# Kernel tuning notes

Hardware: AMD Instinct MI355X
Metric: run time of the kernel (lower is better)

Reference implementation:

```python
import jax, jax.numpy as jnp
import numpy as np

MODEL_DIM = 512
NUM_HEADS = 8
HEAD_DIM = MODEL_DIM // NUM_HEADS  # 64
NUM_NODE = 1024
CLUSTER = 128
S = 60
EMBED = 0.5


def setup_inputs() -> dict:
    key = jax.random.key(0)
    ks = jax.random.split(key, 16)
    d = MODEL_DIM
    sc = 1.0 / np.sqrt(d)
    inp = {
        "x": jax.random.normal(ks[0], (4, 12, NUM_NODE, d), dtype=jnp.float32),
        "Wq": jax.random.normal(ks[1], (d, d), dtype=jnp.float32) * sc,
        "bq": jnp.zeros((d,), jnp.float32),
        "Wk": jax.random.normal(ks[2], (d, d), dtype=jnp.float32) * sc,
        "bk": jnp.zeros((d,), jnp.float32),
        "Wv": jax.random.normal(ks[3], (d, d), dtype=jnp.float32) * sc,
        "bv": jnp.zeros((d,), jnp.float32),
        "We": jax.random.normal(ks[4], (d, d), dtype=jnp.float32) * sc,
        "be": jnp.zeros((d,), jnp.float32),
        "Wo": jax.random.normal(ks[5], (d, d), dtype=jnp.float32) * sc,
        "bo": jnp.zeros((d,), jnp.float32),
        # adp_pos is initialized to zeros in torch; use small randn for a non-degenerate test
        "adp_pos": jax.random.normal(ks[6], (NUM_NODE, CLUSTER), dtype=jnp.float32) * 0.02,
        "U1": jax.random.normal(ks[7], (HEAD_DIM, S), dtype=jnp.float32) * np.sqrt(2.0 / (HEAD_DIM + S)),
        "U2": jax.random.normal(ks[8], (S, HEAD_DIM), dtype=jnp.float32) * np.sqrt(2.0 / (S + HEAD_DIM)),
    }
    return inp


def _split_heads(t):
    # torch.cat(torch.split(t, head_dim, -1), 0): heads stacked head-major on batch dim
    return jnp.concatenate(jnp.split(t, NUM_HEADS, axis=-1), axis=0)


def _merge_heads(t):
    return jnp.concatenate(jnp.split(t, NUM_HEADS, axis=0), axis=-1)


def _pool_nodes(t):
    # AdaptiveAvgPool2d((CLUSTER, None)) on (B,T,N,D) with N % CLUSTER == 0 -> block mean
    B, T, N, D = t.shape
    return t.reshape(B, T, CLUSTER, N // CLUSTER, D).mean(axis=3)


def reference(x, Wq, bq, Wk, bk, Wv, bv, We, be, Wo, bo, adp_pos, U1, U2):
    q = x @ Wq.T + bq                      # (B,T,N,D)
    k = _pool_nodes(x @ Wk.T + bk)          # (B,T,C,D)
    v = _pool_nodes(x @ Wv.T + bv)          # (B,T,C,D)
    ev = x @ We.T + be                      # (B,T,N,D)

    qh = _split_heads(q)                    # (B*H,T,N,d)
    kh = _split_heads(k)                    # (B*H,T,C,d)
    vh = _split_heads(v)                    # (B*H,T,C,d)
    evh = _split_heads(ev)                  # (B*H,T,N,d)

    # external attention branch: softmax over node dim (-2)
    exa = jax.nn.softmax(evh @ U1, axis=-2)  # (B*H,T,N,S)
    exa_val = (exa @ U2) * EMBED + evh       # (B*H,T,N,d)

    score = jnp.einsum("btnd,btcd->btnc", qh, kh) / np.sqrt(HEAD_DIM)
    score = score + adp_pos[None, None]      # (B*H,T,N,C)
    attn = jax.nn.softmax(score, axis=-1)

    out = attn @ vh + exa_val                # (B*H,T,N,d)
    out = _merge_heads(out)                  # (B,T,N,D)
    return out @ Wo.T + bo
```

## Files before the change

kernel.cpp:

```cpp
#include <hip/hip_runtime.h>


#define LOG2E 1.44269504088896f

typedef __attribute__((ext_vector_type(4))) float f32x4;
typedef __attribute__((ext_vector_type(8))) short bf16x8;

__device__ __forceinline__ unsigned short f2bf(float f) {
    union { float f; unsigned u; } v; v.f = f;
    unsigned r = (v.u + 0x7fffu + ((v.u >> 16) & 1u)) >> 16;
    return (unsigned short)r;
}
__device__ __forceinline__ float bf2f(unsigned short h) {
    union { unsigned u; float f; } v; v.u = ((unsigned)h) << 16;
    return v.f;
}
__device__ __forceinline__ unsigned cvt_pk_bf16(float lo, float hi) {
    unsigned r;
    asm("v_cvt_pk_bf16_f32 %0, %1, %2" : "=v"(r) : "v"(lo), "v"(hi));
    return r;
}
__device__ __forceinline__ void gll16(const void* g, void* l) {
    __builtin_amdgcn_global_load_lds((const __attribute__((address_space(1))) void*)g,
                                     (__attribute__((address_space(3))) void*)l,
                                     16, 0, 0);
}

__global__ void cvt_w(const float* __restrict__ Wq, const float* __restrict__ Wk,
                      const float* __restrict__ Wv, const float* __restrict__ We,
                      const float* __restrict__ Wo, const float* __restrict__ U1,
                      const float* __restrict__ U2,
                      const float* __restrict__ bq, const float* __restrict__ bk,
                      const float* __restrict__ bv, const float* __restrict__ be,
                      unsigned short* __restrict__ Wqe, unsigned short* __restrict__ Wkv,
                      unsigned short* __restrict__ Wob, unsigned short* __restrict__ U1T,
                      unsigned short* __restrict__ U2bT,
                      float* __restrict__ bqe, float* __restrict__ bkv)
{
    int i = blockIdx.x * 256 + threadIdx.x;
    if (i < 524288) {
        int r = i >> 9;
        float v = (r < 512) ? Wq[i] * 0.125f : We[i - 262144];
        Wqe[i] = f2bf(v);
    } else if (i < 1048576) {
        int j = i - 524288; int r = j >> 9;
        float v = (r < 512) ? Wk[j] : Wv[j - 262144];
        Wkv[j] = f2bf(v);
    } else if (i < 1310720) {
        int j = i - 1048576;
        Wob[j] = f2bf(Wo[j]);
    } else if (i < 1314816) {
        int j = i - 1310720; int s = j >> 6, k = j & 63;
        U1T[j] = (s < 60) ? f2bf(U1[k * 60 + s] * LOG2E) : (unsigned short)0;
    } else if (i < 1318912) {
        int j = i - 1314816; int d = j >> 6, s = j & 63;
        U2bT[j] = (s < 60) ? f2bf(U2[s * 64 + d] * 0.5f) : (unsigned short)0;
    } else if (i < 1319936) {
        int j = i - 1318912;
        bqe[j] = (j < 512) ? bq[j] * 0.125f : be[j - 512];
    } else if (i < 1320960) {
        int j = i - 1319936;
        bkv[j] = (j < 512) ? bk[j] : bv[j - 512];
    }
}

__global__ void cvt_pool(const float* __restrict__ x, unsigned short* __restrict__ xb,
                         unsigned short* __restrict__ xpb)
{
    int i = blockIdx.x * 256 + threadIdx.x;
    int d4 = i & 127;
    int btc = i >> 7;
    int bt = btc >> 7, c = btc & 127;
    long base = ((long)(bt * 1024 + c * 8)) * 128 + d4;
    const float4* src = (const float4*)x + base;
    ushort4* dst = (ushort4*)xb + base;
    float sx = 0.f, sy = 0.f, sz = 0.f, sw = 0.f;
#pragma unroll
    for (int j = 0; j < 8; j++) {
        float4 v = src[(long)j * 128];
        sx += v.x; sy += v.y; sz += v.z; sw += v.w;
        ushort4 o;
        o.x = f2bf(v.x); o.y = f2bf(v.y); o.z = f2bf(v.z); o.w = f2bf(v.w);
        dst[(long)j * 128] = o;
    }
    ushort4 p;
    p.x = f2bf(sx * 0.125f); p.y = f2bf(sy * 0.125f);
    p.z = f2bf(sz * 0.125f); p.w = f2bf(sw * 0.125f);
    ((ushort4*)xpb)[(long)btc * 128 + d4] = p;
}

__global__ __launch_bounds__(256, 4) void g1_qev(
    const unsigned short* __restrict__ A, const unsigned short* __restrict__ W,
    const float* __restrict__ bias, unsigned short* __restrict__ qh,
    unsigned short* __restrict__ evh)
{
    const int K = 512;
    __shared__ __attribute__((aligned(16))) unsigned short As[128 * 32];
    __shared__ __attribute__((aligned(16))) unsigned short Bs[128 * 32];
    const int tid = threadIdx.x;
    const int wave = tid >> 6, lane = tid & 63;
    const int quad = lane >> 4, l16 = lane & 15;
    const int b = blockIdx.x, xcd = b & 7, j = b >> 3;
    const int m0 = (((j >> 3) << 3) + xcd) * 128, n0 = (j & 7) * 128;
    const int wm = (wave & 1) * 64, wn = (wave >> 1) * 64;

    f32x4 acc[4][4];
#pragma unroll
    for (int i = 0; i < 4; i++)
#pragma unroll
        for (int jj = 0; jj < 4; jj++) acc[i][jj] = (f32x4){0.f, 0.f, 0.f, 0.f};

    const int c0 = tid, c1 = tid + 256;
    const int r0 = c0 >> 2, kc0 = (c0 & 3) * 8;
    const int r1 = c1 >> 2, kc1 = (c1 & 3) * 8;
    const unsigned short* pa0 = A + (long)(m0 + r0) * K + kc0;
    const unsigned short* pa1 = A + (long)(m0 + r1) * K + kc1;
    const unsigned short* pb0 = W + (long)(n0 + r0) * K + kc0;
    const unsigned short* pb1 = W + (long)(n0 + r1) * K + kc1;
    unsigned short* lA0 = &As[wave * 512];
    unsigned short* lA1 = &As[2048 + wave * 512];
    unsigned short* lB0 = &Bs[wave * 512];
    unsigned short* lB1 = &Bs[2048 + wave * 512];

    for (int k0 = 0; k0 < K; k0 += 32) {
        gll16(pa0 + k0, lA0);
        gll16(pa1 + k0, lA1);
        gll16(pb0 + k0, lB0);
        gll16(pb1 + k0, lB1);
        __syncthreads();
        bf16x8 af[4], bfr[4];
#pragma unroll
        for (int t = 0; t < 4; t++)
            af[t] = *(const bf16x8*)&As[(wm + t * 16 + l16) * 32 + quad * 8];
#pragma unroll
        for (int t = 0; t < 4; t++)
            bfr[t] = *(const bf16x8*)&Bs[(wn + t * 16 + l16) * 32 + quad * 8];
#pragma unroll
        for (int tm = 0; tm < 4; tm++)
#pragma unroll
            for (int tn = 0; tn < 4; tn++)
                acc[tm][tn] = __builtin_amdgcn_mfma_f32_16x16x32_bf16(
                    af[tm], bfr[tn], acc[tm][tn], 0, 0, 0);
        __syncthreads();
    }

#pragma unroll
    for (int tm = 0; tm < 4; tm++)
#pragma unroll
        for (int tn = 0; tn < 4; tn++) {
            int cc = n0 + wn + tn * 16 + l16;
            float bv = bias[cc];
            int hq = (cc >> 6) & 7, dd = cc & 63;
            int rr0 = m0 + wm + tm * 16 + quad * 4;
            int bt = rr0 >> 10, n = rr0 & 1023;
            unsigned short* dst = ((cc < 512) ? qh : evh)
                + ((long)(bt * 8 + hq) * 1024 + n) * 64 + dd;
#pragma unroll
            for (int r = 0; r < 4; r++)
                dst[(long)r * 64] = f2bf(acc[tm][tn][r] + bv);
        }
}

template <int NTL2>
__global__ __launch_bounds__(256, 4) void gemm_bt(
    const unsigned short* __restrict__ A, const unsigned short* __restrict__ W,
    const float* __restrict__ bias, float* __restrict__ Cout,
    int N, int K)
{
    __shared__ __attribute__((aligned(16))) unsigned short As[128 * 32];
    __shared__ __attribute__((aligned(16))) unsigned short Bs[128 * 32];
    const int tid = threadIdx.x;
    const int wave = tid >> 6, lane = tid & 63;
    const int quad = lane >> 4, l16 = lane & 15;
    const int b = blockIdx.x, xcd = b & 7, j = b >> 3;
    const int m0 = (((j >> NTL2) << 3) + xcd) * 128;
    const int n0 = (j & ((1 << NTL2) - 1)) * 128;
    const int wm = (wave & 1) * 64, wn = (wave >> 1) * 64;

    f32x4 acc[4][4];
#pragma unroll
    for (int i = 0; i < 4; i++)
#pragma unroll
        for (int jj = 0; jj < 4; jj++) acc[i][jj] = (f32x4){0.f, 0.f, 0.f, 0.f};

    const int c0 = tid, c1 = tid + 256;
    const int r0 = c0 >> 2, kc0 = (c0 & 3) * 8;
    const int r1 = c1 >> 2, kc1 = (c1 & 3) * 8;
    const unsigned short* pa0 = A + (long)(m0 + r0) * K + kc0;
    const unsigned short* pa1 = A + (long)(m0 + r1) * K + kc1;
    const unsigned short* pb0 = W + (long)(n0 + r0) * K + kc0;
    const unsigned short* pb1 = W + (long)(n0 + r1) * K + kc1;
    unsigned short* lA0 = &As[wave * 512];
    unsigned short* lA1 = &As[2048 + wave * 512];
    unsigned short* lB0 = &Bs[wave * 512];
    unsigned short* lB1 = &Bs[2048 + wave * 512];

    for (int k0 = 0; k0 < K; k0 += 32) {
        gll16(pa0 + k0, lA0);
        gll16(pa1 + k0, lA1);
        gll16(pb0 + k0, lB0);
        gll16(pb1 + k0, lB1);
        __syncthreads();
        bf16x8 af[4], bfr[4];
#pragma unroll
        for (int t = 0; t < 4; t++)
            af[t] = *(const bf16x8*)&As[(wm + t * 16 + l16) * 32 + quad * 8];
#pragma unroll
        for (int t = 0; t < 4; t++)
            bfr[t] = *(const bf16x8*)&Bs[(wn + t * 16 + l16) * 32 + quad * 8];
#pragma unroll
        for (int tm = 0; tm < 4; tm++)
#pragma unroll
            for (int tn = 0; tn < 4; tn++)
                acc[tm][tn] = __builtin_amdgcn_mfma_f32_16x16x32_bf16(
                    af[tm], bfr[tn], acc[tm][tn], 0, 0, 0);
        __syncthreads();
    }

#pragma unroll
    for (int tm = 0; tm < 4; tm++)
#pragma unroll
        for (int tn = 0; tn < 4; tn++) {
            int cc = n0 + wn + tn * 16 + l16;
            float bv = bias[cc];
#pragma unroll
            for (int r = 0; r < 4; r++) {
                int rr = m0 + wm + tm * 16 + quad * 4 + r;
                Cout[(long)rr * N + cc] = acc[tm][tn][r] + bv;
            }
        }
}

__global__ __launch_bounds__(256, 4) void g2_kv(
    const unsigned short* __restrict__ A, const unsigned short* __restrict__ W,
    const float* __restrict__ bias, unsigned short* __restrict__ kvK,
    unsigned short* __restrict__ vT)
{
    const int K = 512;
    __shared__ __attribute__((aligned(16))) unsigned short As[128 * 32];
    __shared__ __attribute__((aligned(16))) unsigned short Bs[128 * 32];
    const int tid = threadIdx.x;
    const int wave = tid >> 6, lane = tid & 63;
    const int quad = lane >> 4, l16 = lane & 15;
    const int b = blockIdx.x, xcd = b & 7, j = b >> 3;
    const int m0 = (((j >> 3) << 3) + xcd) * 128, n0 = (j & 7) * 128;
    const int wm = (wave & 1) * 64, wn = (wave >> 1) * 64;

    f32x4 acc[4][4];
#pragma unroll
    for (int i = 0; i < 4; i++)
#pragma unroll
        for (int jj = 0; jj < 4; jj++) acc[i][jj] = (f32x4){0.f, 0.f, 0.f, 0.f};

    const int c0 = tid, c1 = tid + 256;
    const int r0 = c0 >> 2, kc0 = (c0 & 3) * 8;
    const int r1 = c1 >> 2, kc1 = (c1 & 3) * 8;
    const unsigned short* pa0 = A + (long)(m0 + r0) * K + kc0;
    const unsigned short* pa1 = A + (long)(m0 + r1) * K + kc1;
    const unsigned short* pb0 = W + (long)(n0 + r0) * K + kc0;
    const unsigned short* pb1 = W + (long)(n0 + r1) * K + kc1;
    unsigned short* lA0 = &As[wave * 512];
    unsigned short* lA1 = &As[2048 + wave * 512];
    unsigned short* lB0 = &Bs[wave * 512];
    unsigned short* lB1 = &Bs[2048 + wave * 512];

    for (int k0 = 0; k0 < K; k0 += 32) {
        gll16(pa0 + k0, lA0);
        gll16(pa1 + k0, lA1);
        gll16(pb0 + k0, lB0);
        gll16(pb1 + k0, lB1);
        __syncthreads();
        bf16x8 af[4], bfr[4];
#pragma unroll
        for (int t = 0; t < 4; t++)
            af[t] = *(const bf16x8*)&As[(wm + t * 16 + l16) * 32 + quad * 8];
#pragma unroll
        for (int t = 0; t < 4; t++)
            bfr[t] = *(const bf16x8*)&Bs[(wn + t * 16 + l16) * 32 + quad * 8];
#pragma unroll
        for (int tm = 0; tm < 4; tm++)
#pragma unroll
            for (int tn = 0; tn < 4; tn++)
                acc[tm][tn] = __builtin_amdgcn_mfma_f32_16x16x32_bf16(
                    af[tm], bfr[tn], acc[tm][tn], 0, 0, 0);
        __syncthreads();
    }

#pragma unroll
    for (int tm = 0; tm < 4; tm++)
#pragma unroll
        for (int tn = 0; tn < 4; tn++) {
            int cc = n0 + wn + tn * 16 + l16;
            float bv = bias[cc];
            int rrb = m0 + wm + tm * 16 + quad * 4;
            if (cc < 512) {
#pragma unroll
                for (int r = 0; r < 4; r++)
                    kvK[(long)(rrb + r) * 512 + cc] = f2bf(acc[tm][tn][r] + bv);
            } else {
                int hh = (cc - 512) >> 6, dd = (cc - 512) & 63;
                int btv = rrb >> 7, cv = rrb & 127;
                ushort4 o;
                o.x = f2bf(acc[tm][tn][0] + bv);
                o.y = f2bf(acc[tm][tn][1] + bv);
                o.z = f2bf(acc[tm][tn][2] + bv);
                o.w = f2bf(acc[tm][tn][3] + bv);
                *(ushort4*)(vT + ((long)(btv * 8 + hh) * 64 + dd) * 128 + cv) = o;
            }
        }
}

__global__ __launch_bounds__(256, 4) void ez_kernel(
    const unsigned short* __restrict__ evh, const unsigned short* __restrict__ U1T,
    float* __restrict__ pM, float* __restrict__ pL)
{
    __shared__ float ms4[4][64];
    __shared__ float ls4[4][64];
    int tid = threadIdx.x, bx = blockIdx.x;
    int bt = bx >> 6, h = (bx >> 3) & 7, nb = bx & 7;
    int wave = tid >> 6, lane = tid & 63, quad = lane >> 4, l16 = lane & 15;
    long gb0 = (long)(bt * 8 + h) * 1024 + nb * 128;

    f32x4 acc[2][4];
#pragma unroll
    for (int i = 0; i < 2; i++)
#pragma unroll
        for (int t = 0; t < 4; t++) acc[i][t] = (f32x4){0.f, 0.f, 0.f, 0.f};

#pragma unroll
    for (int kt = 0; kt < 2; kt++) {
        bf16x8 a[2], b[4];
#pragma unroll
        for (int i = 0; i < 2; i++)
            a[i] = *(const bf16x8*)(evh + (gb0 + (wave * 2 + i) * 16 + l16) * 64
                                    + kt * 32 + quad * 8);
#pragma unroll
        for (int t = 0; t < 4; t++)
            b[t] = *(const bf16x8*)(U1T + (t * 16 + l16) * 64 + kt * 32 + quad * 8);
#pragma unroll
        for (int i = 0; i < 2; i++)
#pragma unroll
            for (int t = 0; t < 4; t++)
                acc[i][t] = __builtin_amdgcn_mfma_f32_16x16x32_bf16(a[i], b[t], acc[i][t], 0, 0, 0);
    }

    float mp[4], lp[4];
#pragma unroll
    for (int t = 0; t < 4; t++) {
        float m = -1e30f;
#pragma unroll
        for (int i = 0; i < 2; i++)
#pragma unroll
            for (int r = 0; r < 4; r++) m = fmaxf(m, acc[i][t][r]);
        float l = 0.f;
#pragma unroll
        for (int i = 0; i < 2; i++)
#pragma unroll
            for (int r = 0; r < 4; r++) l += exp2f(acc[i][t][r] - m);
        mp[t] = m; lp[t] = l;
    }
#pragma unroll
    for (int d = 16; d <= 32; d <<= 1)
#pragma unroll
        for (int t = 0; t < 4; t++) {
            float mo = __shfl_xor(mp[t], d, 64);
            float lo = __shfl_xor(lp[t], d, 64);
            float nm = fmaxf(mp[t], mo);
            lp[t] = lp[t] * exp2f(mp[t] - nm) + lo * exp2f(mo - nm);
            mp[t] = nm;
        }
    if (quad == 0) {
#pragma unroll
        for (int t = 0; t < 4; t++) {
            ms4[wave][t * 16 + l16] = mp[t];
            ls4[wave][t * 16 + l16] = lp[t];
        }
    }
    __syncthreads();
    if (tid < 64) {
        float M = ms4[0][tid];
#pragma unroll
        for (int w = 1; w < 4; w++) M = fmaxf(M, ms4[w][tid]);
        float L = 0.f;
#pragma unroll
        for (int w = 0; w < 4; w++) L += ls4[w][tid] * exp2f(ms4[w][tid] - M);
        pM[(long)bx * 64 + tid] = M;
        pL[(long)bx * 64 + tid] = L;
    }
}

__global__ void es_reduce(const float* __restrict__ pM, const float* __restrict__ pL,
                          float* __restrict__ dS)
{
    int g = blockIdx.x, s = threadIdx.x;
    float mv[8], lv[8], M = -1e30f;
#pragma unroll
    for (int nb = 0; nb < 8; nb++) {
        mv[nb] = pM[(long)(g * 8 + nb) * 64 + s];
        lv[nb] = pL[(long)(g * 8 + nb) * 64 + s];
        M = fmaxf(M, mv[nb]);
    }
    float L = 0.f;
#pragma unroll
    for (int nb = 0; nb < 8; nb++) L += lv[nb] * exp2f(mv[nb] - M);
    dS[(long)g * 64 + s] = (s < 60) ? (M + __log2f(L)) : 1e30f;
}

__global__ __launch_bounds__(256, 4) void att_kernel(
    const unsigned short* __restrict__ qh, const unsigned short* __restrict__ evh,
    const unsigned short* __restrict__ kvK, const unsigned short* __restrict__ vT,
    const float* __restrict__ dS, const float* __restrict__ adp,
    const unsigned short* __restrict__ U1T, const unsigned short* __restrict__ U2bT,
    unsigned short* __restrict__ attn_out)
{
    __shared__ __attribute__((aligned(16))) unsigned short Ps[128 * 136];

    int tid = threadIdx.x, bx = blockIdx.x;
    int bt = bx >> 6, h = (bx >> 3) & 7, nb = bx & 7;
    int wave = tid >> 6, lane = tid & 63, quad = lane >> 4, l16 = lane & 15;
    int n0 = nb * 128;
    const int g = bt * 8 + h;
    const long grow0 = (long)g * 1024 + n0;

    f32x4 sc[2][8];
#pragma unroll
    for (int i = 0; i < 2; i++)
#pragma unroll
        for (int t = 0; t < 8; t++) sc[i][t] = (f32x4){0.f, 0.f, 0.f, 0.f};

#pragma unroll
    for (int kt = 0; kt < 2; kt++) {
        bf16x8 qf[2];
#pragma unroll
        for (int i = 0; i < 2; i++)
            qf[i] = *(const bf16x8*)(qh + (grow0 + wave * 32 + i * 16 + l16) * 64
                                     + kt * 32 + quad * 8);
#pragma unroll
        for (int tn = 0; tn < 8; tn++) {
            bf16x8 kf = *(const bf16x8*)(kvK + (long)(bt * 128 + tn * 16 + l16) * 512
                                         + h * 64 + kt * 32 + quad * 8);
#pragma unroll
            for (int i = 0; i < 2; i++)
                sc[i][tn] = __builtin_amdgcn_mfma_f32_16x16x32_bf16(kf, qf[i], sc[i][tn], 0, 0, 0);
        }
    }

#pragma unroll
    for (int i = 0; i < 2; i++) {
        const int qr = wave * 32 + i * 16 + l16;
        float m = -1e30f;
#pragma unroll
        for (int tn = 0; tn < 8; tn++) {
            float4 ad = *(const float4*)(adp + (long)(n0 + qr) * 128 + tn * 16 + quad * 4);
            sc[i][tn][0] += ad.x; sc[i][tn][1] += ad.y;
            sc[i][tn][2] += ad.z; sc[i][tn][3] += ad.w;
#pragma unroll
            for (int r = 0; r < 4; r++) m = fmaxf(m, sc[i][tn][r]);
        }
        m = fmaxf(m, __shfl_xor(m, 16, 64));
        m = fmaxf(m, __shfl_xor(m, 32, 64));
        float s = 0.f;
#pragma unroll
        for (int tn = 0; tn < 8; tn++)
#pragma unroll
            for (int r = 0; r < 4; r++) {
                float p = exp2f((sc[i][tn][r] - m) * LOG2E);
                sc[i][tn][r] = p; s += p;
            }
        s += __shfl_xor(s, 16, 64);
        s += __shfl_xor(s, 32, 64);
        float rinv = 1.0f / s;
#pragma unroll
        for (int tn = 0; tn < 8; tn++) {
            uint2 w2;
            w2.x = cvt_pk_bf16(sc[i][tn][0] * rinv, sc[i][tn][1] * rinv);
            w2.y = cvt_pk_bf16(sc[i][tn][2] * rinv, sc[i][tn][3] * rinv);
            *(uint2*)&Ps[qr * 136 + tn * 16 + quad * 4] = w2;
        }
    }

    f32x4 za[2][4];
#pragma unroll
    for (int i = 0; i < 2; i++)
#pragma unroll
        for (int t = 0; t < 4; t++) za[i][t] = (f32x4){0.f, 0.f, 0.f, 0.f};
#pragma unroll
    for (int kt = 0; kt < 2; kt++) {
        bf16x8 u1f[4], evf[2];
#pragma unroll
        for (int t = 0; t < 4; t++)
            u1f[t] = *(const bf16x8*)(U1T + (t * 16 + l16) * 64 + kt * 32 + quad * 8);
#pragma unroll
        for (int i = 0; i < 2; i++)
            evf[i] = *(const bf16x8*)(evh + (grow0 + wave * 32 + i * 16 + l16) * 64
                                      + kt * 32 + quad * 8);
#pragma unroll
        for (int i = 0; i < 2; i++)
#pragma unroll
            for (int t = 0; t < 4; t++)
                za[i][t] = __builtin_amdgcn_mfma_f32_16x16x32_bf16(u1f[t], evf[i], za[i][t], 0, 0, 0);
    }
    float4 dv[4];
#pragma unroll
    for (int t = 0; t < 4; t++)
        dv[t] = *(const float4*)(dS + (long)g * 64 + t * 16 + quad * 4);

    f32x4 oc[2][4];
#pragma unroll
    for (int i = 0; i < 2; i++)
#pragma unroll
        for (int t = 0; t < 4; t++) oc[i][t] = (f32x4){0.f, 0.f, 0.f, 0.f};

#pragma unroll
    for (int kt = 0; kt < 4; kt++) {
        bf16x8 a[2];
#pragma unroll
        for (int i = 0; i < 2; i++)
            a[i] = *(const bf16x8*)&Ps[(wave * 32 + i * 16 + l16) * 136 + kt * 32 + quad * 8];
#pragma unroll
        for (int tn = 0; tn < 4; tn++) {
            bf16x8 b = *(const bf16x8*)(vT + ((long)g * 64 + tn * 16 + l16) * 128
                                        + kt * 32 + quad * 8);
#pragma unroll
            for (int i = 0; i < 2; i++)
                oc[i][tn] = __builtin_amdgcn_mfma_f32_16x16x32_bf16(a[i], b, oc[i][tn], 0, 0, 0);
        }
    }

#pragma unroll
    for (int i = 0; i < 2; i++) {
        const int row = wave * 32 + i * 16 + l16;
#pragma unroll
        for (int t = 0; t < 4; t++) {
            float e0 = exp2f(za[i][t][0] - dv[t].x);
            float e1 = exp2f(za[i][t][1] - dv[t].y);
            float e2 = exp2f(za[i][t][2] - dv[t].z);
            float e3 = exp2f(za[i][t][3] - dv[t].w);
            uint2 w2;
            w2.x = cvt_pk_bf16(e0, e1);
            w2.y = cvt_pk_bf16(e2, e3);
            *(uint2*)&Ps[row * 136 + t * 16 + quad * 4] = w2;
        }
    }

#pragma unroll
    for (int kt = 0; kt < 2; kt++) {
        bf16x8 eaf[2];
#pragma unroll
        for (int i = 0; i < 2; i++)
            eaf[i] = *(const bf16x8*)&Ps[(wave * 32 + i * 16 + l16) * 136 + kt * 32 + quad * 8];
#pragma unroll
        for (int tn = 0; tn < 4; tn++) {
            bf16x8 b = *(const bf16x8*)(U2bT + (tn * 16 + l16) * 64 + kt * 32 + quad * 8);
#pragma unroll
            for (int i = 0; i < 2; i++)
                oc[i][tn] = __builtin_amdgcn_mfma_f32_16x16x32_bf16(eaf[i], b, oc[i][tn], 0, 0, 0);
        }
    }

#pragma unroll
    for (int i = 0; i < 2; i++)
#pragma unroll
        for (int tn = 0; tn < 4; tn++)
#pragma unroll
            for (int r = 0; r < 4; r++) {
                int rr = wave * 32 + i * 16 + quad * 4 + r;
                int cc = tn * 16 + l16;
                float ev = bf2f(evh[(grow0 + rr) * 64 + cc]);
                attn_out[((long)bt * 1024 + n0 + rr) * 512 + h * 64 + cc]
                    = f2bf(oc[i][tn][r] + ev);
            }
}

extern "C" void kernel_launch(void* const* d_in, const int* in_sizes, int n_in,
                              void* d_out, int out_size, void* d_ws, size_t ws_size,
                              hipStream_t stream)
{
    const float* x   = (const float*)d_in[0];
    const float* Wq  = (const float*)d_in[1];
    const float* bq  = (const float*)d_in[2];
    const float* Wk  = (const float*)d_in[3];
    const float* bk  = (const float*)d_in[4];
    const float* Wv  = (const float*)d_in[5];
    const float* bv  = (const float*)d_in[6];
    const float* We  = (const float*)d_in[7];
    const float* be  = (const float*)d_in[8];
    const float* Wo  = (const float*)d_in[9];
    const float* bo  = (const float*)d_in[10];
    const float* adp = (const float*)d_in[11];
    const float* U1  = (const float*)d_in[12];
    const float* U2  = (const float*)d_in[13];

    char* ws = (char*)d_ws;
    unsigned short* xb   = (unsigned short*)(ws + 0);
    unsigned short* aout = xb;
    float*          pMb  = (float*)(ws + 0);
    float*          pLb  = (float*)(ws + 786432);
    unsigned short* xpb  = (unsigned short*)(ws + 50331648);
    unsigned short* qh   = (unsigned short*)(ws + 56623104);
    unsigned short* evh  = (unsigned short*)(ws + 106954752);
    unsigned short* kvK  = (unsigned short*)(ws + 157286400);
    unsigned short* vT   = (unsigned short*)(ws + 163577856);
    float*          dSb  = (float*)(ws + 169869312);
    unsigned short* Wqe  = (unsigned short*)(ws + 217055232);
    unsigned short* Wkv  = (unsigned short*)(ws + 218103808);
    unsigned short* Wob  = (unsigned short*)(ws + 219152384);
    unsigned short* U1T  = (unsigned short*)(ws + 219676672);
    unsigned short* U2bT = (unsigned short*)(ws + 219684864);
    float*          bqe  = (float*)(ws + 219877376);
    float*          bkv  = (float*)(ws + 219881472);

    cvt_w<<<5160, 256, 0, stream>>>(Wq, Wk, Wv, We, Wo, U1, U2, bq, bk, bv, be,
                                    Wqe, Wkv, Wob, U1T, U2bT, bqe, bkv);
    cvt_pool<<<3072, 256, 0, stream>>>(x, xb, xpb);

    g1_qev<<<3072, 256, 0, stream>>>(xb, Wqe, bqe, qh, evh);
    g2_kv<<<384, 256, 0, stream>>>(xpb, Wkv, bkv, kvK, vT);

    ez_kernel<<<3072, 256, 0, stream>>>(evh, U1T, pMb, pLb);
    es_reduce<<<384, 64, 0, stream>>>(pMb, pLb, dSb);
    att_kernel<<<3072, 256, 0, stream>>>(qh, evh, kvK, vT, dSb, adp, U1T, U2bT, aout);

    gemm_bt<2><<<1536, 256, 0, stream>>>(aout, Wob, bo, (float*)d_out, 512, 512);
}
```

Before: 446.1 us.

## Double GEMM K-tile to 64 with XOR-swizzled LDS and hoist evh loads

The three bf16 GEMM kernels now stage a 64-wide K tile per iteration instead of 32. This halves the number of barrier pairs and loop iterations. An XOR swizzle on the column chunk, applied both in the global-to-LDS load addressing and the fragment reads, is meant to avoid LDS bank conflicts from the wider 128-byte rows. The attention kernel now issues its evh fragment loads earlier, before the softmax, so their latency overlaps with that work. In exchange LDS use per block doubles, which may cut occupancy, and the early loads keep more registers live.

Measured after the change: 463.8 us. 1.04x slower.

```diff
diff --git a/kernel.cpp b/kernel.cpp
--- a/kernel.cpp
+++ b/kernel.cpp
@@ -89,14 +89,15 @@
     ((ushort4*)xpb)[(long)btc * 128 + d4] = p;
 }
 
+
 __global__ __launch_bounds__(256, 4) void g1_qev(
     const unsigned short* __restrict__ A, const unsigned short* __restrict__ W,
     const float* __restrict__ bias, unsigned short* __restrict__ qh,
     unsigned short* __restrict__ evh)
 {
     const int K = 512;
-    __shared__ __attribute__((aligned(16))) unsigned short As[128 * 32];
-    __shared__ __attribute__((aligned(16))) unsigned short Bs[128 * 32];
+    __shared__ __attribute__((aligned(16))) unsigned short As[128 * 64];
+    __shared__ __attribute__((aligned(16))) unsigned short Bs[128 * 64];
     const int tid = threadIdx.x;
     const int wave = tid >> 6, lane = tid & 63;
     const int quad = lane >> 4, l16 = lane & 15;
@@ -110,37 +111,49 @@
 #pragma unroll
         for (int jj = 0; jj < 4; jj++) acc[i][jj] = (f32x4){0.f, 0.f, 0.f, 0.f};
 
-    const int c0 = tid, c1 = tid + 256;
-    const int r0 = c0 >> 2, kc0 = (c0 & 3) * 8;
-    const int r1 = c1 >> 2, kc1 = (c1 & 3) * 8;
-    const unsigned short* pa0 = A + (long)(m0 + r0) * K + kc0;
-    const unsigned short* pa1 = A + (long)(m0 + r1) * K + kc1;
-    const unsigned short* pb0 = W + (long)(n0 + r0) * K + kc0;
-    const unsigned short* pb1 = W + (long)(n0 + r1) * K + kc1;
+    const int rr0 = tid >> 3;
+    const int kcs = ((tid & 7) ^ ((tid >> 3) & 7)) * 8;
+    const unsigned short* pa0 = A + (long)(m0 + rr0) * K + kcs;
+    const unsigned short* pa1 = A + (long)(m0 + 32 + rr0) * K + kcs;
+    const unsigned short* pa2 = A + (long)(m0 + 64 + rr0) * K + kcs;
+    const unsigned short* pa3 = A + (long)(m0 + 96 + rr0) * K + kcs;
+    const unsigned short* pb0 = W + (long)(n0 + rr0) * K + kcs;
+    const unsigned short* pb1 = W + (long)(n0 + 32 + rr0) * K + kcs;
+    const unsigned short* pb2 = W + (long)(n0 + 64 + rr0) * K + kcs;
+    const unsigned short* pb3 = W + (long)(n0 + 96 + rr0) * K + kcs;
     unsigned short* lA0 = &As[wave * 512];
     unsigned short* lA1 = &As[2048 + wave * 512];
+    unsigned short* lA2 = &As[4096 + wave * 512];
+    unsigned short* lA3 = &As[6144 + wave * 512];
     unsigned short* lB0 = &Bs[wave * 512];
     unsigned short* lB1 = &Bs[2048 + wave * 512];
-
-    for (int k0 = 0; k0 < K; k0 += 32) {
-        gll16(pa0 + k0, lA0);
-        gll16(pa1 + k0, lA1);
-        gll16(pb0 + k0, lB0);
-        gll16(pb1 + k0, lB1);
+    unsigned short* lB2 = &Bs[4096 + wave * 512];
+    unsigned short* lB3 = &Bs[6144 + wave * 512];
+    const int rswz = (l16 & 7) * 8;
+
+    for (int k0 = 0; k0 < K; k0 += 64) {
+        gll16(pa0 + k0, lA0); gll16(pa1 + k0, lA1);
+        gll16(pa2 + k0, lA2); gll16(pa3 + k0, lA3);
+        gll16(pb0 + k0, lB0); gll16(pb1 + k0, lB1);
+        gll16(pb2 + k0, lB2); gll16(pb3 + k0, lB3);
         __syncthreads();
-        bf16x8 af[4], bfr[4];
-#pragma unroll
-        for (int t = 0; t < 4; t++)
-            af[t] = *(const bf16x8*)&As[(wm + t * 16 + l16) * 32 + quad * 8];
-#pragma unroll
-        for (int t = 0; t < 4; t++)
-            bfr[t] = *(const bf16x8*)&Bs[(wn + t * 16 + l16) * 32 + quad * 8];
-#pragma unroll
-        for (int tm = 0; tm < 4; tm++)
-#pragma unroll
-            for (int tn = 0; tn < 4; tn++)
-                acc[tm][tn] = __builtin_amdgcn_mfma_f32_16x16x32_bf16(
-                    af[tm], bfr[tn], acc[tm][tn], 0, 0, 0);
+#pragma unroll
+        for (int kt = 0; kt < 2; kt++) {
+            const int kc = (kt * 32 + quad * 8) ^ rswz;
+            bf16x8 af[4], bfr[4];
+#pragma unroll
+            for (int t = 0; t < 4; t++)
+                af[t] = *(const bf16x8*)&As[(wm + t * 16 + l16) * 64 + kc];
+#pragma unroll
+            for (int t = 0; t < 4; t++)
+                bfr[t] = *(const bf16x8*)&Bs[(wn + t * 16 + l16) * 64 + kc];
+#pragma unroll
+            for (int tm = 0; tm < 4; tm++)
+#pragma unroll
+                for (int tn = 0; tn < 4; tn++)
+                    acc[tm][tn] = __builtin_amdgcn_mfma_f32_16x16x32_bf16(
+                        af[tm], bfr[tn], acc[tm][tn], 0, 0, 0);
+        }
         __syncthreads();
     }
 
@@ -151,8 +164,8 @@
             int cc = n0 + wn + tn * 16 + l16;
             float bv = bias[cc];
             int hq = (cc >> 6) & 7, dd = cc & 63;
-            int rr0 = m0 + wm + tm * 16 + quad * 4;
-            int bt = rr0 >> 10, n = rr0 & 1023;
+            int rrb = m0 + wm + tm * 16 + quad * 4;
+            int bt = rrb >> 10, n = rrb & 1023;
             unsigned short* dst = ((cc < 512) ? qh : evh)
                 + ((long)(bt * 8 + hq) * 1024 + n) * 64 + dd;
 #pragma unroll
@@ -167,8 +180,8 @@
     const float* __restrict__ bias, float* __restrict__ Cout,
     int N, int K)
 {
-    __shared__ __attribute__((aligned(16))) unsigned short As[128 * 32];
-    __shared__ __attribute__((aligned(16))) unsigned short Bs[128 * 32];
+    __shared__ __attribute__((aligned(16))) unsigned short As[128 * 64];
+    __shared__ __attribute__((aligned(16))) unsigned short Bs[128 * 64];
     const int tid = threadIdx.x;
     const int wave = tid >> 6, lane = tid & 63;
     const int quad = lane >> 4, l16 = lane & 15;
@@ -183,37 +196,49 @@
 #pragma unroll
         for (int jj = 0; jj < 4; jj++) acc[i][jj] = (f32x4){0.f, 0.f, 0.f, 0.f};
 
-    const int c0 = tid, c1 = tid + 256;
-    const int r0 = c0 >> 2, kc0 = (c0 & 3) * 8;
-    const int r1 = c1 >> 2, kc1 = (c1 & 3) * 8;
-    const unsigned short* pa0 = A + (long)(m0 + r0) * K + kc0;
-    const unsigned short* pa1 = A + (long)(m0 + r1) * K + kc1;
-    const unsigned short* pb0 = W + (long)(n0 + r0) * K + kc0;
-    const unsigned short* pb1 = W + (long)(n0 + r1) * K + kc1;
+    const int rr0 = tid >> 3;
+    const int kcs = ((tid & 7) ^ ((tid >> 3) & 7)) * 8;
+    const unsigned short* pa0 = A + (long)(m0 + rr0) * K + kcs;
+    const unsigned short* pa1 = A + (long)(m0 + 32 + rr0) * K + kcs;
+    const unsigned short* pa2 = A + (long)(m0 + 64 + rr0) * K + kcs;
+    const unsigned short* pa3 = A + (long)(m0 + 96 + rr0) * K + kcs;
+    const unsigned short* pb0 = W + (long)(n0 + rr0) * K + kcs;
+    const unsigned short* pb1 = W + (long)(n0 + 32 + rr0) * K + kcs;
+    const unsigned short* pb2 = W + (long)(n0 + 64 + rr0) * K + kcs;
+    const unsigned short* pb3 = W + (long)(n0 + 96 + rr0) * K + kcs;
     unsigned short* lA0 = &As[wave * 512];
     unsigned short* lA1 = &As[2048 + wave * 512];
+    unsigned short* lA2 = &As[4096 + wave * 512];
+    unsigned short* lA3 = &As[6144 + wave * 512];
     unsigned short* lB0 = &Bs[wave * 512];
     unsigned short* lB1 = &Bs[2048 + wave * 512];
-
-    for (int k0 = 0; k0 < K; k0 += 32) {
-        gll16(pa0 + k0, lA0);
-        gll16(pa1 + k0, lA1);
-        gll16(pb0 + k0, lB0);
-        gll16(pb1 + k0, lB1);
+    unsigned short* lB2 = &Bs[4096 + wave * 512];
+    unsigned short* lB3 = &Bs[6144 + wave * 512];
+    const int rswz = (l16 & 7) * 8;
+
+    for (int k0 = 0; k0 < K; k0 += 64) {
+        gll16(pa0 + k0, lA0); gll16(pa1 + k0, lA1);
+        gll16(pa2 + k0, lA2); gll16(pa3 + k0, lA3);
+        gll16(pb0 + k0, lB0); gll16(pb1 + k0, lB1);
+        gll16(pb2 + k0, lB2); gll16(pb3 + k0, lB3);
         __syncthreads();
-        bf16x8 af[4], bfr[4];
-#pragma unroll
-        for (int t = 0; t < 4; t++)
-            af[t] = *(const bf16x8*)&As[(wm + t * 16 + l16) * 32 + quad * 8];
-#pragma unroll
-        for (int t = 0; t < 4; t++)
-            bfr[t] = *(const bf16x8*)&Bs[(wn + t * 16 + l16) * 32 + quad * 8];
-#pragma unroll
-        for (int tm = 0; tm < 4; tm++)
-#pragma unroll
-            for (int tn = 0; tn < 4; tn++)
-                acc[tm][tn] = __builtin_amdgcn_mfma_f32_16x16x32_bf16(
-                    af[tm], bfr[tn], acc[tm][tn], 0, 0, 0);
+#pragma unroll
+        for (int kt = 0; kt < 2; kt++) {
+            const int kc = (kt * 32 + quad * 8) ^ rswz;
+            bf16x8 af[4], bfr[4];
+#pragma unroll
+            for (int t = 0; t < 4; t++)
+                af[t] = *(const bf16x8*)&As[(wm + t * 16 + l16) * 64 + kc];
+#pragma unroll
+            for (int t = 0; t < 4; t++)
+                bfr[t] = *(const bf16x8*)&Bs[(wn + t * 16 + l16) * 64 + kc];
+#pragma unroll
+            for (int tm = 0; tm < 4; tm++)
+#pragma unroll
+                for (int tn = 0; tn < 4; tn++)
+                    acc[tm][tn] = __builtin_amdgcn_mfma_f32_16x16x32_bf16(
+                        af[tm], bfr[tn], acc[tm][tn], 0, 0, 0);
+        }
         __syncthreads();
     }
 
@@ -237,8 +262,8 @@
     unsigned short* __restrict__ vT)
 {
     const int K = 512;
-    __shared__ __attribute__((aligned(16))) unsigned short As[128 * 32];
-    __shared__ __attribute__((aligned(16))) unsigned short Bs[128 * 32];
+    __shared__ __attribute__((aligned(16))) unsigned short As[128 * 64];
+    __shared__ __attribute__((aligned(16))) unsigned short Bs[128 * 64];
     const int tid = threadIdx.x;
     const int wave = tid >> 6, lane = tid & 63;
     const int quad = lane >> 4, l16 = lane & 15;
@@ -252,37 +277,49 @@
 #pragma unroll
         for (int jj = 0; jj < 4; jj++) acc[i][jj] = (f32x4){0.f, 0.f, 0.f, 0.f};
 
-    const int c0 = tid, c1 = tid + 256;
-    const int r0 = c0 >> 2, kc0 = (c0 & 3) * 8;
-    const int r1 = c1 >> 2, kc1 = (c1 & 3) * 8;
-    const unsigned short* pa0 = A + (long)(m0 + r0) * K + kc0;
-    const unsigned short* pa1 = A + (long)(m0 + r1) * K + kc1;
-    const unsigned short* pb0 = W + (long)(n0 + r0) * K + kc0;
-    const unsigned short* pb1 = W + (long)(n0 + r1) * K + kc1;
+    const int rr0 = tid >> 3;
+    const int kcs = ((tid & 7) ^ ((tid >> 3) & 7)) * 8;
+    const unsigned short* pa0 = A + (long)(m0 + rr0) * K + kcs;
+    const unsigned short* pa1 = A + (long)(m0 + 32 + rr0) * K + kcs;
+    const unsigned short* pa2 = A + (long)(m0 + 64 + rr0) * K + kcs;
+    const unsigned short* pa3 = A + (long)(m0 + 96 + rr0) * K + kcs;
+    const unsigned short* pb0 = W + (long)(n0 + rr0) * K + kcs;
+    const unsigned short* pb1 = W + (long)(n0 + 32 + rr0) * K + kcs;
+    const unsigned short* pb2 = W + (long)(n0 + 64 + rr0) * K + kcs;
+    const unsigned short* pb3 = W + (long)(n0 + 96 + rr0) * K + kcs;
     unsigned short* lA0 = &As[wave * 512];
     unsigned short* lA1 = &As[2048 + wave * 512];
+    unsigned short* lA2 = &As[4096 + wave * 512];
+    unsigned short* lA3 = &As[6144 + wave * 512];
     unsigned short* lB0 = &Bs[wave * 512];
     unsigned short* lB1 = &Bs[2048 + wave * 512];
-
-    for (int k0 = 0; k0 < K; k0 += 32) {
-        gll16(pa0 + k0, lA0);
-        gll16(pa1 + k0, lA1);
-        gll16(pb0 + k0, lB0);
-        gll16(pb1 + k0, lB1);
+    unsigned short* lB2 = &Bs[4096 + wave * 512];
+    unsigned short* lB3 = &Bs[6144 + wave * 512];
+    const int rswz = (l16 & 7) * 8;
+
+    for (int k0 = 0; k0 < K; k0 += 64) {
+        gll16(pa0 + k0, lA0); gll16(pa1 + k0, lA1);
+        gll16(pa2 + k0, lA2); gll16(pa3 + k0, lA3);
+        gll16(pb0 + k0, lB0); gll16(pb1 + k0, lB1);
+        gll16(pb2 + k0, lB2); gll16(pb3 + k0, lB3);
         __syncthreads();
-        bf16x8 af[4], bfr[4];
-#pragma unroll
-        for (int t = 0; t < 4; t++)
-            af[t] = *(const bf16x8*)&As[(wm + t * 16 + l16) * 32 + quad * 8];
-#pragma unroll
-        for (int t = 0; t < 4; t++)
-            bfr[t] = *(const bf16x8*)&Bs[(wn + t * 16 + l16) * 32 + quad * 8];
-#pragma unroll
-        for (int tm = 0; tm < 4; tm++)
-#pragma unroll
-            for (int tn = 0; tn < 4; tn++)
-                acc[tm][tn] = __builtin_amdgcn_mfma_f32_16x16x32_bf16(
-                    af[tm], bfr[tn], acc[tm][tn], 0, 0, 0);
+#pragma unroll
+        for (int kt = 0; kt < 2; kt++) {
+            const int kc = (kt * 32 + quad * 8) ^ rswz;
+            bf16x8 af[4], bfr[4];
+#pragma unroll
+            for (int t = 0; t < 4; t++)
+                af[t] = *(const bf16x8*)&As[(wm + t * 16 + l16) * 64 + kc];
+#pragma unroll
+            for (int t = 0; t < 4; t++)
+                bfr[t] = *(const bf16x8*)&Bs[(wn + t * 16 + l16) * 64 + kc];
+#pragma unroll
+            for (int tm = 0; tm < 4; tm++)
+#pragma unroll
+                for (int tn = 0; tn < 4; tn++)
+                    acc[tm][tn] = __builtin_amdgcn_mfma_f32_16x16x32_bf16(
+                        af[tm], bfr[tn], acc[tm][tn], 0, 0, 0);
+        }
         __syncthreads();
     }
 
@@ -445,6 +482,14 @@
         }
     }
 
+    bf16x8 evf[2][2];
+#pragma unroll
+    for (int kt = 0; kt < 2; kt++)
+#pragma unroll
+        for (int i = 0; i < 2; i++)
+            evf[kt][i] = *(const bf16x8*)(evh + (grow0 + wave * 32 + i * 16 + l16) * 64
+                                          + kt * 32 + quad * 8);
+
 #pragma unroll
     for (int i = 0; i < 2; i++) {
         const int qr = wave * 32 + i * 16 + l16;
@@ -486,19 +531,15 @@
         for (int t = 0; t < 4; t++) za[i][t] = (f32x4){0.f, 0.f, 0.f, 0.f};
 #pragma unroll
     for (int kt = 0; kt < 2; kt++) {
-        bf16x8 u1f[4], evf[2];
+        bf16x8 u1f[4];
 #pragma unroll
         for (int t = 0; t < 4; t++)
             u1f[t] = *(const bf16x8*)(U1T + (t * 16 + l16) * 64 + kt * 32 + quad * 8);
 #pragma unroll
         for (int i = 0; i < 2; i++)
-            evf[i] = *(const bf16x8*)(evh + (grow0 + wave * 32 + i * 16 + l16) * 64
-                                      + kt * 32 + quad * 8);
-#pragma unroll
-        for (int i = 0; i < 2; i++)
-#pragma unroll
-            for (int t = 0; t < 4; t++)
-                za[i][t] = __builtin_amdgcn_mfma_f32_16x16x32_bf16(u1f[t], evf[i], za[i][t], 0, 0, 0);
+#pragma unroll
+            for (int t = 0; t < 4; t++)
+                za[i][t] = __builtin_amdgcn_mfma_f32_16x16x32_bf16(u1f[t], evf[kt][i], za[i][t], 0, 0, 0);
     }
     float4 dv[4];
 #pragma unroll
```
